# Optimization experiments

Measured on AMD Instinct MI355X. Metric: run time of the kernel, lower is better.

Reference implementation:

```python
import jax, jax.numpy as jnp
import numpy as np

DIM = 2048
HEADS = 16
HEAD_DIM = 128
KV_HEADS = 8
ROPE_BASE = 10000.0


def _rope_tables(seq_len):
    inv_freq = 1.0 / (ROPE_BASE ** (jnp.arange(0, HEAD_DIM, 2, dtype=jnp.float32) / HEAD_DIM))
    t = jnp.arange(seq_len, dtype=jnp.float32)
    freqs = jnp.outer(t, inv_freq)              # [S, D/2]
    emb = jnp.concatenate([freqs, freqs], -1)    # [S, D]
    return jnp.cos(emb), jnp.sin(emb)


def _rotate_half(x):
    x1, x2 = jnp.split(x, 2, axis=-1)
    return jnp.concatenate([-x2, x1], axis=-1)


def setup_inputs() -> dict:
    key = jax.random.key(0)
    ks = jax.random.split(key, 5)
    B, S = 2, 2048
    s = 0.02
    return {
        "x": jax.random.normal(ks[0], (B, S, DIM), jnp.float32),
        "Wq": jax.random.normal(ks[1], (DIM, HEADS * HEAD_DIM), jnp.float32) * s,
        "Wk": jax.random.normal(ks[2], (DIM, KV_HEADS * HEAD_DIM), jnp.float32) * s,
        "Wv": jax.random.normal(ks[3], (DIM, KV_HEADS * HEAD_DIM), jnp.float32) * s,
        "Wo": jax.random.normal(ks[4], (HEADS * HEAD_DIM, DIM), jnp.float32) * s,
    }


def reference(x, Wq, Wk, Wv, Wo):
    B, S, _ = x.shape
    scale = 1.0 / np.sqrt(HEAD_DIM).astype(np.float32)
    q = (x @ Wq).reshape(B, S, HEADS, HEAD_DIM)
    k = (x @ Wk).reshape(B, S, KV_HEADS, HEAD_DIM)
    v = (x @ Wv).reshape(B, S, KV_HEADS, HEAD_DIM)
    cos, sin = _rope_tables(S)                   # [S, D]
    cos = cos[None, :, None, :]                  # broadcast over batch, heads
    sin = sin[None, :, None, :]
    q = q * cos + _rotate_half(q) * sin
    k = k * cos + _rotate_half(k) * sin
    q = jnp.transpose(q, (0, 2, 1, 3))           # [B,H,S,D]
    k = jnp.transpose(k, (0, 2, 1, 3))           # [B,Hkv,S,D]
    v = jnp.transpose(v, (0, 2, 1, 3))
    rep = HEADS // KV_HEADS
    k = jnp.repeat(k, rep, axis=1)               # GQA -> [B,H,S,D]
    v = jnp.repeat(v, rep, axis=1)
    scores = jnp.einsum('bhid,bhjd->bhij', q, k) * scale
    causal = jnp.tril(jnp.ones((S, S), dtype=bool))
    scores = jnp.where(causal, scores, -jnp.inf)
    attn = jax.nn.softmax(scores, axis=-1)
    out = jnp.einsum('bhij,bhjd->bhid', attn, v)
    out = jnp.transpose(out, (0, 2, 1, 3)).reshape(B, S, HEADS * HEAD_DIM)
    return out @ Wo
```

## Files before the change

### kernel.cpp

```cpp
#include <hip/hip_runtime.h>

#define DIMX 2048
#define SEQ  2048
#define BATCH 2
#define NH   16
#define NKV  8
#define HD   128
#define MTOK (BATCH*SEQ)
#define NQKV 4096
#define QKLD 3072

typedef __bf16 bf16x8 __attribute__((ext_vector_type(8)));
typedef float  f32x4  __attribute__((ext_vector_type(4)));
typedef float  f32x16 __attribute__((ext_vector_type(16)));
typedef unsigned short u16x8 __attribute__((ext_vector_type(8)));
typedef unsigned short u16x4 __attribute__((ext_vector_type(4)));
typedef unsigned int   u32x4 __attribute__((ext_vector_type(4)));

__device__ __forceinline__ unsigned short f2bf(float f) {
    unsigned u = __builtin_bit_cast(unsigned, f);
    u += 0x7fffu + ((u >> 16) & 1u);
    return (unsigned short)(u >> 16);
}
__device__ __forceinline__ float bf2f(unsigned short h) {
    unsigned u = ((unsigned)h) << 16;
    return __builtin_bit_cast(float, u);
}

__device__ __forceinline__ void gload16(const void* g, void* l) {
    __builtin_amdgcn_global_load_lds(
        (const __attribute__((address_space(1))) unsigned int*)g,
        (__attribute__((address_space(3))) unsigned int*)l, 16, 0, 0);
}

__global__ __launch_bounds__(256) void k_convert(const float* __restrict__ in,
                                                 unsigned short* __restrict__ out, int n8) {
    int i = blockIdx.x * 256 + threadIdx.x;
    if (i >= n8) return;
    f32x4 a = ((const f32x4*)in)[(size_t)i*2];
    f32x4 b = ((const f32x4*)in)[(size_t)i*2+1];
    u16x8 o;
    o[0]=f2bf(a[0]); o[1]=f2bf(a[1]); o[2]=f2bf(a[2]); o[3]=f2bf(a[3]);
    o[4]=f2bf(b[0]); o[5]=f2bf(b[1]); o[6]=f2bf(b[2]); o[7]=f2bf(b[3]);
    ((u16x8*)out)[i] = o;
}

__global__ __launch_bounds__(256) void k_transpose(const float* __restrict__ W,
                                                   unsigned short* __restrict__ Wt,
                                                   int K, int N) {
    __shared__ unsigned short tile[64*65];
    int t = threadIdx.x;
    int n0 = blockIdx.x * 64, k0 = blockIdx.y * 64;
    #pragma unroll
    for (int i = 0; i < 16; ++i) {
        int idx = t + i*256, r = idx >> 6, c = idx & 63;
        tile[r*65+c] = f2bf(W[(size_t)(k0+r)*N + n0 + c]);
    }
    __syncthreads();
    #pragma unroll
    for (int i = 0; i < 16; ++i) {
        int idx = t + i*256, n = idx >> 6, k = idx & 63;
        Wt[(size_t)(n0+n)*K + k0 + k] = tile[k*65+n];
    }
}

template<int NREP, int MODE>
__global__ __launch_bounds__(512, 2) void k_gemm256(const unsigned short* __restrict__ A,
                                                    const unsigned short* __restrict__ Bt,
                                                    void* __restrict__ Cv,
                                                    unsigned short* __restrict__ Vt,
                                                    int M, int N, int K, int ldc) {
    constexpr int BN  = NREP * 64;
    constexpr int BWC = NREP * 16;
    constexpr int NLD = 4 + NREP;
    __shared__ __align__(16) char As[2][32768];
    __shared__ __align__(16) char Bs[2][BN * 128];
    int bid = blockIdx.x;
    int rem = (bid & 7) * 32 + (bid >> 3);
    int bx = rem & 15, by = rem >> 4;
    int row0 = by * 256, col0 = bx * BN;
    int tid = threadIdx.x, wave = tid >> 6, lane = tid & 63;
    int wr = wave >> 2, wc = wave & 3;
    int g = lane >> 4, r16 = lane & 15;
    const char* Ab = (const char*)A;
    const char* Bb = (const char*)Bt;

    f32x4 acc[8][NREP] = {};

    auto STAGE = [&](int buf, int t) {
        int k0b = t * 128;
        #pragma unroll
        for (int p = 0; p < 4; ++p) {
            int c = wave * 4 + p;
            int o = c * 1024 + lane * 16;
            int row = o >> 7;
            int colb = (o & 127) ^ ((row & 7) << 4);
            gload16(Ab + (size_t)(row0 + row) * (size_t)(K * 2) + k0b + colb, &As[buf][c * 1024]);
        }
        #pragma unroll
        for (int p = 0; p < NREP; ++p) {
            int c = wave * NREP + p;
            int o = c * 1024 + lane * 16;
            int row = o >> 7;
            int colb = (o & 127) ^ ((row & 7) << 4);
            gload16(Bb + (size_t)(col0 + row) * (size_t)(K * 2) + k0b + colb, &Bs[buf][c * 1024]);
        }
    };

    int nt = K >> 6;
    STAGE(0, 0);
    STAGE(1, 1);
    if constexpr (NREP == 4) asm volatile("s_waitcnt vmcnt(8)" ::: "memory");
    else                     asm volatile("s_waitcnt vmcnt(6)" ::: "memory");
    __builtin_amdgcn_s_barrier();

    for (int t = 0; t < nt; ++t) {
        int buf = t & 1;
        const char* AL = As[buf];
        const char* BL = Bs[buf];
        bf16x8 a0[4][2], a1[4][2], bfr[NREP][2];
        #pragma unroll
        for (int mi = 0; mi < 4; ++mi)
            #pragma unroll
            for (int s = 0; s < 2; ++s) {
                int r = wr*128 + mi*16 + r16;
                int o = r*128 + s*64 + g*16;
                a0[mi][s] = *(const bf16x8*)(AL + (o ^ ((r & 7) << 4)));
            }
        #pragma unroll
        for (int ni = 0; ni < NREP; ++ni)
            #pragma unroll
            for (int s = 0; s < 2; ++s) {
                int r = wc*BWC + ni*16 + r16;
                int o = r*128 + s*64 + g*16;
                bfr[ni][s] = *(const bf16x8*)(BL + (o ^ ((r & 7) << 4)));
            }
        __builtin_amdgcn_s_setprio(1);
        #pragma unroll
        for (int mi = 0; mi < 4; ++mi)
            #pragma unroll
            for (int ni = 0; ni < NREP; ++ni)
                #pragma unroll
                for (int s = 0; s < 2; ++s)
                    acc[mi][ni] = __builtin_amdgcn_mfma_f32_16x16x32_bf16(a0[mi][s], bfr[ni][s], acc[mi][ni], 0, 0, 0);
        __builtin_amdgcn_s_setprio(0);
        #pragma unroll
        for (int mi = 0; mi < 4; ++mi)
            #pragma unroll
            for (int s = 0; s < 2; ++s) {
                int r = wr*128 + 64 + mi*16 + r16;
                int o = r*128 + s*64 + g*16;
                a1[mi][s] = *(const bf16x8*)(AL + (o ^ ((r & 7) << 4)));
            }
        asm volatile("s_waitcnt lgkmcnt(0)" ::: "memory");
        __builtin_amdgcn_sched_barrier(0);
        __builtin_amdgcn_s_barrier();
        if (t + 2 < nt) STAGE(buf, t + 2);
        __builtin_amdgcn_sched_barrier(0);
        __builtin_amdgcn_s_setprio(1);
        #pragma unroll
        for (int mi = 0; mi < 4; ++mi)
            #pragma unroll
            for (int ni = 0; ni < NREP; ++ni)
                #pragma unroll
                for (int s = 0; s < 2; ++s)
                    acc[mi+4][ni] = __builtin_amdgcn_mfma_f32_16x16x32_bf16(a1[mi][s], bfr[ni][s], acc[mi+4][ni], 0, 0, 0);
        __builtin_amdgcn_s_setprio(0);
        if (t + 2 < nt) {
            if constexpr (NREP == 4) asm volatile("s_waitcnt vmcnt(8)" ::: "memory");
            else                     asm volatile("s_waitcnt vmcnt(6)" ::: "memory");
        } else {
            asm volatile("s_waitcnt vmcnt(0)" ::: "memory");
        }
        __builtin_amdgcn_s_barrier();
    }

    #pragma unroll
    for (int mi = 0; mi < 8; ++mi)
        #pragma unroll
        for (int ni = 0; ni < NREP; ++ni) {
            if (MODE == 0 && col0 >= 3072) {
                int vcol = col0 + wc*BWC + ni*16 + r16 - 3072;
                int d = vcol & 127, kh = vcol >> 7;
                int row = row0 + wr*128 + mi*16 + g*4;
                int b = row >> 11, s = row & (SEQ-1);
                u16x4 pk;
                #pragma unroll
                for (int rr = 0; rr < 4; ++rr) pk[rr] = f2bf(acc[mi][ni][rr]);
                *(u16x4*)&Vt[((size_t)(b*NKV + kh)*HD + d)*SEQ + s] = pk;
            } else {
                #pragma unroll
                for (int rr = 0; rr < 4; ++rr) {
                    int row = row0 + wr*128 + mi*16 + g*4 + rr;
                    int col = col0 + wc*BWC + ni*16 + r16;
                    float v = acc[mi][ni][rr];
                    if (MODE == 1) ((float*)Cv)[(size_t)row*ldc + col] = v;
                    else ((unsigned short*)Cv)[(size_t)row*ldc + col] = f2bf(v);
                }
            }
        }
}

__global__ __launch_bounds__(256) void k_rope(unsigned short* __restrict__ qkv) {
    int tid = blockIdx.x * 256 + threadIdx.x;
    int i    = tid & 63;
    int rest = tid >> 6;
    int head = rest % (NH + NKV);
    int tok  = rest / (NH + NKV);
    int pos  = tok & (SEQ - 1);
    size_t base = (size_t)tok * QKLD + head*HD;
    float x1 = bf2f(qkv[base + i]);
    float x2 = bf2f(qkv[base + i + 64]);
    float inv = exp2f(-0.20762050593046014f * (float)i);
    float ang = (float)pos * inv;
    float s, c;
    sincosf(ang, &s, &c);
    qkv[base + i]      = f2bf(x1*c - x2*s);
    qkv[base + i + 64] = f2bf(x2*c + x1*s);
}

__global__ __launch_bounds__(256, 2) void k_attn(const unsigned short* __restrict__ qkv,
                                                 const unsigned short* __restrict__ Vt,
                                                 unsigned short* __restrict__ attn_out) {
    __shared__ __align__(16) char KsB[2][16384];
    __shared__ __align__(16) char VsB[2][16384];
    int bid = blockIdx.x;
    int xcd = bid & 7, slot = bid >> 3;
    int bh  = xcd * 4 + (slot >> 4);
    int xx  = slot & 15;
    int qt  = (slot & 32) ? (15 - xx) : xx;
    int b = bh >> 4, h = bh & 15;
    int kvh = h >> 1;
    int tid = threadIdx.x, wave = tid >> 6, lane = tid & 63;
    int l31 = lane & 31, hi = lane >> 5;
    int q0w = qt * 128 + wave * 32;
    int qg  = q0w + l31;
    const unsigned short* qbase = qkv + (size_t)(b * SEQ) * QKLD;
    const char* kbase = (const char*)(qbase + DIMX + kvh * HD);
    const char* vbase = (const char*)(Vt + ((size_t)(b * NKV + kvh) * HD) * SEQ);

    bf16x8 qf[8];
    {
        const unsigned short* qrow = qbase + (size_t)qg * QKLD + h * HD;
        #pragma unroll
        for (int s2 = 0; s2 < 8; ++s2)
            qf[s2] = *(const bf16x8*)(qrow + s2*16 + hi*8);
    }

    f32x16 acc[4] = {};
    float mrow = -1e30f, lrow = 0.f;
    const float SC = 0.08838834764831845f * 1.4426950408889634f;

    auto STAGE = [&](int bsel, int it) {
        int kv0 = it * 64;
        char* KL = KsB[bsel];
        char* VL = VsB[bsel];
        #pragma unroll
        for (int p = 0; p < 4; ++p) {
            int c = wave*4 + p;
            {
                int row  = c*4 + (lane >> 4);
                int colb = ((lane & 15) * 16) ^ ((row & 7) << 4);
                gload16(kbase + (size_t)(kv0 + row) * (QKLD*2) + colb, KL + c*1024);
            }
            {
                int d    = c*8 + (lane >> 3);
                int colb = ((lane & 7) * 16) ^ ((d & 7) << 4);
                gload16(vbase + (size_t)d * (SEQ*2) + (size_t)kv0*2 + colb, VL + c*1024);
            }
        }
    };

    int nt = 2*qt + 2;
    STAGE(0, 0);
    asm volatile("s_waitcnt vmcnt(0)" ::: "memory");
    __syncthreads();

    for (int it = 0; it < nt; ++it) {
        int bsel = it & 1;
        int kv0 = it * 64;
        if (it + 1 < nt) STAGE((it+1) & 1, it + 1);
        if (kv0 <= q0w + 31) {
            const char* KL = KsB[bsel];
            const char* VL = VsB[bsel];
            f32x16 st[2] = {};
            __builtin_amdgcn_s_setprio(1);
            #pragma unroll
            for (int t = 0; t < 2; ++t) {
                int row = t*32 + l31;
                const char* kr = KL + row*256;
                unsigned sw = (unsigned)((row & 7) << 4);
                #pragma unroll
                for (int s2 = 0; s2 < 8; ++s2) {
                    bf16x8 kf = *(const bf16x8*)(kr + (((unsigned)(s2*32 + hi*16)) ^ sw));
                    st[t] = __builtin_amdgcn_mfma_f32_32x32x16_bf16(kf, qf[s2], st[t], 0, 0, 0);
                }
            }
            __builtin_amdgcn_s_setprio(0);
            float mt = -1e30f;
            if (kv0 + 63 <= q0w) {
                #pragma unroll
                for (int t = 0; t < 2; ++t)
                    #pragma unroll
                    for (int r = 0; r < 16; ++r) {
                        float v = st[t][r] * SC;
                        st[t][r] = v; mt = fmaxf(mt, v);
                    }
            } else {
                #pragma unroll
                for (int t = 0; t < 2; ++t)
                    #pragma unroll
                    for (int r = 0; r < 16; ++r) {
                        int kv = kv0 + t*32 + (r & 3) + 8*(r >> 2) + 4*hi;
                        float v = (kv <= qg) ? st[t][r] * SC : -1e30f;
                        st[t][r] = v; mt = fmaxf(mt, v);
                    }
            }
            mt = fmaxf(mt, __shfl_xor(mt, 32, 64));
            if (!__all(mt - mrow <= 8.0f)) {
                float mn = fmaxf(mrow, mt);
                float corr = exp2f(mrow - mn);
                mrow = mn;
                lrow *= corr;
                #pragma unroll
                for (int dt = 0; dt < 4; ++dt)
                    #pragma unroll
                    for (int r = 0; r < 16; ++r) acc[dt][r] *= corr;
            }
            float rs = 0.f;
            #pragma unroll
            for (int t = 0; t < 2; ++t)
                #pragma unroll
                for (int r = 0; r < 16; ++r) {
                    float p = exp2f(st[t][r] - mrow);
                    st[t][r] = p; rs += p;
                }
            rs += __shfl_xor(rs, 32, 64);
            lrow += rs;
            #pragma unroll
            for (int t = 0; t < 2; ++t)
                #pragma unroll
                for (int ks = 0; ks < 2; ++ks) {
                    int rb = ks * 8;
                    float p0 = st[t][rb+0], p1 = st[t][rb+1], p2 = st[t][rb+2], p3 = st[t][rb+3];
                    float p4 = st[t][rb+4], p5 = st[t][rb+5], p6 = st[t][rb+6], p7 = st[t][rb+7];
                    unsigned w0, w1, w2, w3;
                    asm("v_cvt_pk_bf16_f32 %0, %1, %2" : "=v"(w0) : "v"(p0), "v"(p1));
                    asm("v_cvt_pk_bf16_f32 %0, %1, %2" : "=v"(w1) : "v"(p2), "v"(p3));
                    asm("v_cvt_pk_bf16_f32 %0, %1, %2" : "=v"(w2) : "v"(p4), "v"(p5));
                    asm("v_cvt_pk_bf16_f32 %0, %1, %2" : "=v"(w3) : "v"(p6), "v"(p7));
                    asm("v_permlane32_swap_b32 %0, %1" : "+v"(w0), "+v"(w2));
                    asm("v_permlane32_swap_b32 %0, %1" : "+v"(w1), "+v"(w3));
                    u32x4 pu = {w0, w1, w2, w3};
                    bf16x8 pfrag = __builtin_bit_cast(bf16x8, pu);
                    int ks4 = t*2 + ks;
                    __builtin_amdgcn_s_setprio(1);
                    #pragma unroll
                    for (int dt = 0; dt < 4; ++dt) {
                        int d = dt*32 + l31;
                        bf16x8 vf = *(const bf16x8*)(VL + d*128 +
                                     (((unsigned)(ks4*32 + hi*16)) ^ ((unsigned)((d & 7) << 4))));
                        acc[dt] = __builtin_amdgcn_mfma_f32_32x32x16_bf16(vf, pfrag, acc[dt], 0, 0, 0);
                    }
                    __builtin_amdgcn_s_setprio(0);
                }
        }
        asm volatile("s_waitcnt vmcnt(0)" ::: "memory");
        __syncthreads();
    }

    float inv = 1.0f / lrow;
    #pragma unroll
    for (int dt = 0; dt < 4; ++dt)
        #pragma unroll
        for (int qd = 0; qd < 4; ++qd) {
            u16x4 o4;
            #pragma unroll
            for (int j = 0; j < 4; ++j) o4[j] = f2bf(acc[dt][qd*4 + j] * inv);
            int d0 = dt*32 + qd*8 + hi*4;
            *(u16x4*)&attn_out[(size_t)(b*SEQ + qg)*DIMX + h*HD + d0] = o4;
        }
}

extern "C" void kernel_launch(void* const* d_in, const int* in_sizes, int n_in,
                              void* d_out, int out_size, void* d_ws, size_t ws_size,
                              hipStream_t stream) {
    const float* x  = (const float*)d_in[0];
    const float* Wq = (const float*)d_in[1];
    const float* Wk = (const float*)d_in[2];
    const float* Wv = (const float*)d_in[3];
    const float* Wo = (const float*)d_in[4];

    unsigned short* xb   = (unsigned short*)d_ws;
    unsigned short* Wtq  = xb  + (size_t)MTOK*DIMX;
    unsigned short* Wto  = Wtq + (size_t)NQKV*DIMX;
    unsigned short* qkv  = Wto + (size_t)DIMX*DIMX;
    unsigned short* aout = qkv + (size_t)MTOK*QKLD;
    unsigned short* Vt   = aout + (size_t)MTOK*DIMX;

    k_convert<<<(MTOK*DIMX/8 + 255)/256, 256, 0, stream>>>(x, xb, MTOK*DIMX/8);

    dim3 tg32(DIMX/64, DIMX/64);
    dim3 tg16(1024/64, DIMX/64);
    k_transpose<<<tg32, 256, 0, stream>>>(Wq, Wtq,                         DIMX, DIMX);
    k_transpose<<<tg16, 256, 0, stream>>>(Wk, Wtq + (size_t)2048*DIMX,     DIMX, 1024);
    k_transpose<<<tg16, 256, 0, stream>>>(Wv, Wtq + (size_t)3072*DIMX,     DIMX, 1024);
    k_transpose<<<tg32, 256, 0, stream>>>(Wo, Wto,                         DIMX, DIMX);

    k_gemm256<4, 0><<<256, 512, 0, stream>>>(xb, Wtq, qkv, Vt, MTOK, NQKV, DIMX, QKLD);

    k_rope<<<(MTOK*(NH+NKV)*64)/256, 256, 0, stream>>>(qkv);

    k_attn<<<512, 256, 0, stream>>>(qkv, Vt, aout);

    k_gemm256<2, 1><<<256, 512, 0, stream>>>(aout, Wto, (float*)d_out, nullptr, MTOK, DIMX, DIMX, DIMX);
}
```

Measured before the change: 224.8 us.

## Pair causal query tiles per attention block and fold softmax scale into RoPE

Each attention block now handles two query tiles, p and 15-p, one after the other. This gives every block the same 34 KV iterations and halves the grid to 256 blocks, removing the load imbalance from causal masking. The softmax scale and log2e factor are folded into the Q rotation in the RoPE kernel, so the per-score multiply in attention goes away. The cost is Q stored pre-scaled in bf16, which adds rounding, and fewer resident blocks, which lowers occupancy for latency hiding.

```diff
diff --git a/kernel.cpp b/kernel.cpp
--- a/kernel.cpp
+++ b/kernel.cpp
@@ -72,7 +72,6 @@
                                                     int M, int N, int K, int ldc) {
     constexpr int BN  = NREP * 64;
     constexpr int BWC = NREP * 16;
-    constexpr int NLD = 4 + NREP;
     __shared__ __align__(16) char As[2][32768];
     __shared__ __align__(16) char Bs[2][BN * 128];
     int bid = blockIdx.x;
@@ -215,113 +214,111 @@
     float ang = (float)pos * inv;
     float s, c;
     sincosf(ang, &s, &c);
-    qkv[base + i]      = f2bf(x1*c - x2*s);
-    qkv[base + i + 64] = f2bf(x2*c + x1*s);
-}
-
-__global__ __launch_bounds__(256, 2) void k_attn(const unsigned short* __restrict__ qkv,
-                                                 const unsigned short* __restrict__ Vt,
-                                                 unsigned short* __restrict__ attn_out) {
-    __shared__ __align__(16) char KsB[2][16384];
-    __shared__ __align__(16) char VsB[2][16384];
+    float sc = (head < NH) ? 0.12754984523341717f : 1.0f;
+    qkv[base + i]      = f2bf((x1*c - x2*s) * sc);
+    qkv[base + i + 64] = f2bf((x2*c + x1*s) * sc);
+}
+
+__global__ __launch_bounds__(256) void k_attn(const unsigned short* __restrict__ qkv,
+                                              const unsigned short* __restrict__ Vt,
+                                              unsigned short* __restrict__ attn_out) {
+    __shared__ __align__(16) char KVs[2][32768];
     int bid = blockIdx.x;
-    int xcd = bid & 7, slot = bid >> 3;
-    int bh  = xcd * 4 + (slot >> 4);
-    int xx  = slot & 15;
-    int qt  = (slot & 32) ? (15 - xx) : xx;
-    int b = bh >> 4, h = bh & 15;
-    int kvh = h >> 1;
+    int xcd = bid & 7, idx = bid >> 3;
+    int bh  = xcd * 4 + (idx >> 3);
+    int p   = idx & 7;
+    int b = bh >> 4, h = bh & 15, kvh = h >> 1;
     int tid = threadIdx.x, wave = tid >> 6, lane = tid & 63;
     int l31 = lane & 31, hi = lane >> 5;
-    int q0w = qt * 128 + wave * 32;
+    int nt0 = 2*p + 2;
+    constexpr int NT = 34;
+    int q0w = p*128 + wave*32;
     int qg  = q0w + l31;
-    const unsigned short* qbase = qkv + (size_t)(b * SEQ) * QKLD;
-    const char* kbase = (const char*)(qbase + DIMX + kvh * HD);
-    const char* vbase = (const char*)(Vt + ((size_t)(b * NKV + kvh) * HD) * SEQ);
+    const unsigned short* qbase = qkv + (size_t)(b*SEQ)*QKLD;
+    const char* kbase = (const char*)(qbase + DIMX + kvh*HD);
+    const char* vbase = (const char*)(Vt + ((size_t)(b*NKV + kvh)*HD)*SEQ);
 
     bf16x8 qf[8];
-    {
-        const unsigned short* qrow = qbase + (size_t)qg * QKLD + h * HD;
-        #pragma unroll
-        for (int s2 = 0; s2 < 8; ++s2)
-            qf[s2] = *(const bf16x8*)(qrow + s2*16 + hi*8);
-    }
+    auto loadQ = [&](int qrow) {
+        const unsigned short* qr = qbase + (size_t)qrow*QKLD + h*HD;
+        #pragma unroll
+        for (int s2 = 0; s2 < 8; ++s2) qf[s2] = *(const bf16x8*)(qr + s2*16 + hi*8);
+    };
+    loadQ(qg);
 
     f32x16 acc[4] = {};
     float mrow = -1e30f, lrow = 0.f;
-    const float SC = 0.08838834764831845f * 1.4426950408889634f;
-
-    auto STAGE = [&](int bsel, int it) {
-        int kv0 = it * 64;
-        char* KL = KsB[bsel];
-        char* VL = VsB[bsel];
-        #pragma unroll
-        for (int p = 0; p < 4; ++p) {
-            int c = wave*4 + p;
-            {
-                int row  = c*4 + (lane >> 4);
-                int colb = ((lane & 15) * 16) ^ ((row & 7) << 4);
-                gload16(kbase + (size_t)(kv0 + row) * (QKLD*2) + colb, KL + c*1024);
-            }
-            {
-                int d    = c*8 + (lane >> 3);
-                int colb = ((lane & 7) * 16) ^ ((d & 7) << 4);
-                gload16(vbase + (size_t)d * (SEQ*2) + (size_t)kv0*2 + colb, VL + c*1024);
-            }
+
+    auto STAGE = [&](int v, int buf) {
+        int kv0 = (v < nt0 ? v : v - nt0) * 64;
+        char* KL = KVs[buf];
+        char* VL = KL + 16384;
+        #pragma unroll
+        for (int pp = 0; pp < 4; ++pp) {
+            int c = wave*4 + pp;
+            int row  = c*4 + (lane >> 4);
+            int colb = ((lane & 15) * 16) ^ ((row & 7) << 4);
+            gload16(kbase + (size_t)(kv0 + row)*(QKLD*2) + colb, KL + c*1024);
+            int d    = c*8 + (lane >> 3);
+            int colv = ((lane & 7) * 16) ^ ((d & 7) << 4);
+            gload16(vbase + (size_t)d*(SEQ*2) + (size_t)kv0*2 + colv, VL + c*1024);
         }
     };
 
-    int nt = 2*qt + 2;
+    auto writeOut = [&]() {
+        float inv = 1.0f / lrow;
+        #pragma unroll
+        for (int dt = 0; dt < 4; ++dt)
+            #pragma unroll
+            for (int qd = 0; qd < 4; ++qd) {
+                u16x4 o4;
+                #pragma unroll
+                for (int j = 0; j < 4; ++j) o4[j] = f2bf(acc[dt][qd*4 + j] * inv);
+                *(u16x4*)&attn_out[(size_t)(b*SEQ + qg)*DIMX + h*HD + dt*32 + qd*8 + hi*4] = o4;
+            }
+    };
+
     STAGE(0, 0);
     asm volatile("s_waitcnt vmcnt(0)" ::: "memory");
     __syncthreads();
 
-    for (int it = 0; it < nt; ++it) {
-        int bsel = it & 1;
-        int kv0 = it * 64;
-        if (it + 1 < nt) STAGE((it+1) & 1, it + 1);
+    for (int v = 0; v < NT; ++v) {
+        int buf = v & 1;
+        int kv0 = (v < nt0 ? v : v - nt0) * 64;
+        if (v + 1 < NT) STAGE(v + 1, buf ^ 1);
+        const char* KL = KVs[buf];
+        const char* VL = KL + 16384;
         if (kv0 <= q0w + 31) {
-            const char* KL = KsB[bsel];
-            const char* VL = VsB[bsel];
-            f32x16 st[2] = {};
+            f32x16 st0 = {}, st1 = {};
+            const char* kr0 = KL + l31*256;
+            const char* kr1 = KL + (32 + l31)*256;
+            unsigned sw = (unsigned)((l31 & 7) << 4);
             __builtin_amdgcn_s_setprio(1);
             #pragma unroll
-            for (int t = 0; t < 2; ++t) {
-                int row = t*32 + l31;
-                const char* kr = KL + row*256;
-                unsigned sw = (unsigned)((row & 7) << 4);
-                #pragma unroll
-                for (int s2 = 0; s2 < 8; ++s2) {
-                    bf16x8 kf = *(const bf16x8*)(kr + (((unsigned)(s2*32 + hi*16)) ^ sw));
-                    st[t] = __builtin_amdgcn_mfma_f32_32x32x16_bf16(kf, qf[s2], st[t], 0, 0, 0);
+            for (int s2 = 0; s2 < 8; ++s2) {
+                unsigned off = (unsigned)(s2*32 + hi*16);
+                bf16x8 kf0 = *(const bf16x8*)(kr0 + (off ^ sw));
+                bf16x8 kf1 = *(const bf16x8*)(kr1 + (off ^ sw));
+                st0 = __builtin_amdgcn_mfma_f32_32x32x16_bf16(kf0, qf[s2], st0, 0, 0, 0);
+                st1 = __builtin_amdgcn_mfma_f32_32x32x16_bf16(kf1, qf[s2], st1, 0, 0, 0);
+            }
+            __builtin_amdgcn_s_setprio(0);
+            if (kv0 + 63 > q0w) {
+                #pragma unroll
+                for (int r = 0; r < 16; ++r) {
+                    int kvr = kv0 + (r & 3) + 8*(r >> 2) + 4*hi;
+                    st0[r] = (kvr      <= qg) ? st0[r] : -1e30f;
+                    st1[r] = (kvr + 32 <= qg) ? st1[r] : -1e30f;
                 }
             }
-            __builtin_amdgcn_s_setprio(0);
             float mt = -1e30f;
-            if (kv0 + 63 <= q0w) {
-                #pragma unroll
-                for (int t = 0; t < 2; ++t)
-                    #pragma unroll
-                    for (int r = 0; r < 16; ++r) {
-                        float v = st[t][r] * SC;
-                        st[t][r] = v; mt = fmaxf(mt, v);
-                    }
-            } else {
-                #pragma unroll
-                for (int t = 0; t < 2; ++t)
-                    #pragma unroll
-                    for (int r = 0; r < 16; ++r) {
-                        int kv = kv0 + t*32 + (r & 3) + 8*(r >> 2) + 4*hi;
-                        float v = (kv <= qg) ? st[t][r] * SC : -1e30f;
-                        st[t][r] = v; mt = fmaxf(mt, v);
-                    }
-            }
+            #pragma unroll
+            for (int r = 0; r < 16; ++r) { mt = fmaxf(mt, st0[r]); mt = fmaxf(mt, st1[r]); }
             mt = fmaxf(mt, __shfl_xor(mt, 32, 64));
             if (!__all(mt - mrow <= 8.0f)) {
                 float mn = fmaxf(mrow, mt);
                 float corr = exp2f(mrow - mn);
-                mrow = mn;
-                lrow *= corr;
+                mrow = mn; lrow *= corr;
                 #pragma unroll
                 for (int dt = 0; dt < 4; ++dt)
                     #pragma unroll
@@ -329,21 +326,19 @@
             }
             float rs = 0.f;
             #pragma unroll
+            for (int r = 0; r < 16; ++r) {
+                float p0 = exp2f(st0[r] - mrow); st0[r] = p0; rs += p0;
+                float p1 = exp2f(st1[r] - mrow); st1[r] = p1; rs += p1;
+            }
+            lrow += rs + __shfl_xor(rs, 32, 64);
+            #pragma unroll
             for (int t = 0; t < 2; ++t)
                 #pragma unroll
-                for (int r = 0; r < 16; ++r) {
-                    float p = exp2f(st[t][r] - mrow);
-                    st[t][r] = p; rs += p;
-                }
-            rs += __shfl_xor(rs, 32, 64);
-            lrow += rs;
-            #pragma unroll
-            for (int t = 0; t < 2; ++t)
-                #pragma unroll
                 for (int ks = 0; ks < 2; ++ks) {
+                    const f32x16& stt = t ? st1 : st0;
                     int rb = ks * 8;
-                    float p0 = st[t][rb+0], p1 = st[t][rb+1], p2 = st[t][rb+2], p3 = st[t][rb+3];
-                    float p4 = st[t][rb+4], p5 = st[t][rb+5], p6 = st[t][rb+6], p7 = st[t][rb+7];
+                    float p0 = stt[rb+0], p1 = stt[rb+1], p2 = stt[rb+2], p3 = stt[rb+3];
+                    float p4 = stt[rb+4], p5 = stt[rb+5], p6 = stt[rb+6], p7 = stt[rb+7];
                     unsigned w0, w1, w2, w3;
                     asm("v_cvt_pk_bf16_f32 %0, %1, %2" : "=v"(w0) : "v"(p0), "v"(p1));
                     asm("v_cvt_pk_bf16_f32 %0, %1, %2" : "=v"(w1) : "v"(p2), "v"(p3));
@@ -367,19 +362,19 @@
         }
         asm volatile("s_waitcnt vmcnt(0)" ::: "memory");
         __syncthreads();
+        if (v == nt0 - 1) {
+            writeOut();
+            #pragma unroll
+            for (int dt = 0; dt < 4; ++dt)
+                #pragma unroll
+                for (int r = 0; r < 16; ++r) acc[dt][r] = 0.f;
+            mrow = -1e30f; lrow = 0.f;
+            q0w = (15 - p)*128 + wave*32;
+            qg  = q0w + l31;
+            loadQ(qg);
+        }
     }
-
-    float inv = 1.0f / lrow;
-    #pragma unroll
-    for (int dt = 0; dt < 4; ++dt)
-        #pragma unroll
-        for (int qd = 0; qd < 4; ++qd) {
-            u16x4 o4;
-            #pragma unroll
-            for (int j = 0; j < 4; ++j) o4[j] = f2bf(acc[dt][qd*4 + j] * inv);
-            int d0 = dt*32 + qd*8 + hi*4;
-            *(u16x4*)&attn_out[(size_t)(b*SEQ + qg)*DIMX + h*HD + d0] = o4;
-        }
+    writeOut();
 }
 
 extern "C" void kernel_launch(void* const* d_in, const int* in_sizes, int n_in,
@@ -411,7 +406,7 @@
 
     k_rope<<<(MTOK*(NH+NKV)*64)/256, 256, 0, stream>>>(qkv);
 
-    k_attn<<<512, 256, 0, stream>>>(qkv, Vt, aout);
+    k_attn<<<256, 256, 0, stream>>>(qkv, Vt, aout);
 
     k_gemm256<2, 1><<<256, 512, 0, stream>>>(aout, Wto, (float*)d_out, nullptr, MTOK, DIMX, DIMX, DIMX);
 }
```

New measurement: 234.8 us. 4.5% more time.
